# Performance work log

Measured on AMD Instinct MI355X. Metric: run time of the kernel, lower is better.

The kernel has to match this reference:

```python
import jax, jax.numpy as jnp
import numpy as np

# Decode-stage paged attention with ALiBi (HPU flat-PA style):
# batch2block scatter of queries, per-block QK + alibi bias, segment-wise
# stable softmax over each sequence's blocks, AV matmul, block2batch reduce.
BATCH = 32          # decode sequences
H = 32              # query heads
KVH = 8             # kv heads (GQA)
QPK = H // KVH      # queries per kv head
D = 128             # head size
BS = 128            # block size (tokens per KV-cache block)
BLOCKS_PER_SEQ = 16 # context 2048 tokens per sequence
U = BATCH * BLOCKS_PER_SEQ  # 512 used blocks
NB = 600            # total blocks in cache pool
SCALE = 1.0 / float(np.sqrt(D))
NEG = -1e30


def setup_inputs() -> dict:
    key = jax.random.key(0)
    k0, k1, k2 = jax.random.split(key, 3)
    query = jax.random.normal(k0, (BATCH, H, D), jnp.float32)
    key_cache = jax.random.normal(k1, (NB, BS, KVH, D), jnp.float32)
    value_cache = jax.random.normal(k2, (NB, BS, KVH, D), jnp.float32)
    # contiguous PA: used blocks are the first U blocks of the pool
    block_list = jnp.arange(U, dtype=jnp.int32)
    # each sequence owns BLOCKS_PER_SEQ consecutive blocks
    block_groups = (jnp.arange(U, dtype=jnp.int32) // BLOCKS_PER_SEQ).astype(jnp.int32)
    # all blocks fully used (context = BLOCKS_PER_SEQ*BS exactly)
    block_usage = jnp.full((U,), BS, dtype=jnp.int32)
    # alibi_blocks[u, p] = (global position) - (context_len - 1)  (<= 0)
    ctx = BLOCKS_PER_SEQ * BS
    pos = (jnp.arange(U) % BLOCKS_PER_SEQ)[:, None] * BS + jnp.arange(BS)[None, :]
    alibi_blocks = (pos - (ctx - 1)).astype(jnp.float32)
    # standard geometric alibi slopes: 2^(-8*(i+1)/H)
    alibi_slopes = 2.0 ** (-(jnp.arange(1, H + 1, dtype=jnp.float32)) * (8.0 / H))
    return dict(query=query, key_cache=key_cache, value_cache=value_cache,
                alibi_blocks=alibi_blocks, alibi_slopes=alibi_slopes,
                block_list=block_list, block_groups=block_groups,
                block_usage=block_usage)


def reference(query, key_cache, value_cache, alibi_blocks, alibi_slopes,
              block_list, block_groups, block_usage):
    # gather KV blocks from the paged cache
    K = key_cache[block_list]            # [U, BS, KVH, D]
    V = value_cache[block_list]          # [U, BS, KVH, D]
    # batch2block: replicate each sequence's query onto its blocks
    q = query[block_groups] * SCALE      # [U, H, D]
    qg = q.reshape(U, KVH, QPK, D)
    # QK^T per block (GQA: each kv head serves QPK query heads)
    scores = jnp.einsum('ugqd,ukgd->ugqk', qg, K).reshape(U, H, BS)
    # decode alibi bias: [U, H, BS] = alibi_blocks[:,None,:] * slopes[None,:,None]
    scores = scores + alibi_blocks[:, None, :] * alibi_slopes[None, :, None]
    # mask unused slots within each block
    valid = jnp.arange(BS, dtype=jnp.int32)[None, :] < block_usage[:, None]  # [U, BS]
    scores = jnp.where(valid[:, None, :], scores, NEG)
    # stable softmax across all blocks of each sequence (segment-wise)
    bmax = scores.max(-1)                                            # [U, H]
    gmax = jax.ops.segment_max(bmax, block_groups, num_segments=BATCH)
    e = jnp.exp(scores - gmax[block_groups][:, :, None])             # [U, H, BS]
    e = jnp.where(valid[:, None, :], e, 0.0)
    bsum = e.sum(-1)                                                 # [U, H]
    gsum = jax.ops.segment_sum(bsum, block_groups, num_segments=BATCH)  # [B, H]
    # AV per block, then block2batch reduce
    eg = e.reshape(U, KVH, QPK, BS)
    av = jnp.einsum('ugqk,ukgd->ugqd', eg, V).reshape(U, H, D)       # [U, H, D]
    out = jax.ops.segment_sum(av, block_groups, num_segments=BATCH)  # [B, H, D]
    out = out / gsum[:, :, None]
    return out.reshape(BATCH, H * D)
```

## Files before the change

kernel.cpp:

```cpp
#include <hip/hip_runtime.h>
#include <stdint.h>

#define BATCH 32
#define NH    32
#define KVH   8
#define QPK   4
#define DH    128
#define BS    128
#define NEG   (-1e30f)
#define SCALEF 0.08838834764831845f
#define MAXU  512

#define GAS __attribute__((address_space(1)))
#define LAS __attribute__((address_space(3)))

__global__ __launch_bounds__(256, 1)
void pa_alibi_decode(const float* __restrict__ query,
                     const float* __restrict__ key_cache,
                     const float* __restrict__ value_cache,
                     const float* __restrict__ alibi_blocks,
                     const float* __restrict__ alibi_slopes,
                     const int* __restrict__ block_list,
                     const int* __restrict__ block_groups,
                     const int* __restrict__ block_usage,
                     float* __restrict__ out,
                     int U) {
  __shared__ __align__(16) float Kbuf[4][2][32 * DH];
  __shared__ __align__(16) float q_lds[QPK * DH];
  __shared__ __align__(16) float p_lds[4][32 * QPK];
  __shared__ float combO[4][QPK][DH];
  __shared__ float combM[4][QPK];
  __shared__ float combS[4][QPK];
  __shared__ int   ulist[MAXU];
  __shared__ int   pblds[MAXU];
  __shared__ int   uslds[MAXU];
  __shared__ int   ucount;

  const int tid  = threadIdx.x;
  const int w    = tid >> 6;
  const int lane = tid & 63;
  const int r    = lane & 31;
  const int half = lane >> 5;
  const int b    = blockIdx.x >> 3;
  const int g    = blockIdx.x & 7;

  if (w == 0) {
    int cnt = 0;
    for (int base = 0; base < U; base += 64) {
      const int u = base + lane;
      const bool match = (u < U) && (block_groups[u] == b);
      const unsigned long long mk = __ballot(match);
      if (match) {
        const int pre = __popcll(mk & ((1ull << lane) - 1ull));
        ulist[cnt + pre] = u;
      }
      cnt += __popcll(mk);
    }
    if (lane == 0) ucount = cnt;
    for (int i = lane; i < cnt; i += 64) {
      const int u = ulist[i];
      pblds[i] = block_list[u];
      uslds[i] = block_usage[u];
    }
  }

  {
    const float* qsrc = query + ((size_t)b * NH + g * QPK) * DH;
    for (int e = tid; e < QPK * DH; e += 256) q_lds[e] = qsrc[e] * SCALEF;
  }

  float slope[QPK];
#pragma unroll
  for (int qh = 0; qh < QPK; ++qh) slope[qh] = alibi_slopes[g * QPK + qh];

  __syncthreads();

  const int nblk = ucount;

  float m[QPK], s[QPK], O[QPK][4];
#pragma unroll
  for (int qh = 0; qh < QPK; ++qh) {
    m[qh] = NEG; s[qh] = 0.f;
#pragma unroll
    for (int k = 0; k < 4; ++k) O[qh][k] = 0.f;
  }

  int cur = 0;
  int u_cur = 0, pb_cur = 0, us_cur = 0;
  if (nblk > 0) {
    u_cur = ulist[0]; pb_cur = pblds[0]; us_cur = uslds[0];
    const float* base = key_cache + ((size_t)pb_cur * BS + w * 32) * (KVH * DH) + (size_t)g * DH;
    float* buf = &Kbuf[w][0][0];
#pragma unroll
    for (int i = 0; i < 16; ++i) {
      const int t  = 2 * i + half;
      const int sg = r ^ t;
      __builtin_amdgcn_global_load_lds((const GAS void*)(base + (size_t)t * (KVH * DH) + sg * 4),
                                       (LAS void*)(buf + i * 256), 16, 0, 0);
    }
  }

  for (int c = 0; c < nblk; ++c) {
    __builtin_amdgcn_sched_barrier(0);
    asm volatile("s_waitcnt vmcnt(0)" ::: "memory");
    __builtin_amdgcn_sched_barrier(0);

    const float ab = alibi_blocks[(size_t)u_cur * BS + w * 32 + r];
    const bool has_nxt = (c + 1 < nblk);
    int u_nxt = 0, pb_nxt = 0, us_nxt = 0;
    if (has_nxt) { u_nxt = ulist[c + 1]; pb_nxt = pblds[c + 1]; us_nxt = uslds[c + 1]; }

    const float* vb = value_cache + ((size_t)pb_cur * BS + w * 32 + half) * (KVH * DH)
                    + (size_t)g * DH + r * 4;
    float4 vreg[16];
#pragma unroll
    for (int tp = 0; tp < 16; ++tp)
      vreg[tp] = *(const float4*)&vb[(size_t)tp * 2 * (KVH * DH)];

    if (has_nxt) {
      const float* base = key_cache + ((size_t)pb_nxt * BS + w * 32) * (KVH * DH) + (size_t)g * DH;
      float* buf = &Kbuf[w][cur ^ 1][0];
#pragma unroll
      for (int i = 0; i < 16; ++i) {
        const int t  = 2 * i + half;
        const int sg = r ^ t;
        __builtin_amdgcn_global_load_lds((const GAS void*)(base + (size_t)t * (KVH * DH) + sg * 4),
                                         (LAS void*)(buf + i * 256), 16, 0, 0);
      }
    }

    const float* kb = &Kbuf[w][cur][0];
    float acc[QPK] = {0.f, 0.f, 0.f, 0.f};
#pragma unroll
    for (int i = 0; i < 16; ++i) {
      const int j = half * 16 + i;
      const float4 kv = *(const float4*)&kb[r * DH + ((j ^ r) << 2)];
#pragma unroll
      for (int qh = 0; qh < QPK; ++qh) {
        const float4 qv = *(const float4*)&q_lds[qh * DH + (j << 2)];
        acc[qh] += kv.x * qv.x + kv.y * qv.y + kv.z * qv.z + kv.w * qv.w;
      }
    }

    const bool valid = (w * 32 + r) < us_cur;
    float p[QPK];
#pragma unroll
    for (int qh = 0; qh < QPK; ++qh) {
      float sc = acc[qh] + __shfl_xor(acc[qh], 32);
      sc += ab * slope[qh];
      if (!valid) sc = NEG;
      float cm = sc;
#pragma unroll
      for (int off = 1; off < 32; off <<= 1) cm = fmaxf(cm, __shfl_xor(cm, off));
      const float mnew = fmaxf(m[qh], cm);
      const float rs   = __expf(m[qh] - mnew);
      m[qh] = mnew;
      p[qh] = valid ? __expf(sc - mnew) : 0.f;
      s[qh] = s[qh] * rs + (half == 0 ? p[qh] : 0.f);
#pragma unroll
      for (int k = 0; k < 4; ++k) O[qh][k] *= rs;
    }
    if (half == 0)
      *(float4*)&p_lds[w][r * 4] = make_float4(p[0], p[1], p[2], p[3]);

#pragma unroll
    for (int tp = 0; tp < 16; ++tp) {
      const float4 pv = *(const float4*)&p_lds[w][(2 * tp + half) * 4];
      const float4 vv = vreg[tp];
      O[0][0] += pv.x * vv.x; O[0][1] += pv.x * vv.y; O[0][2] += pv.x * vv.z; O[0][3] += pv.x * vv.w;
      O[1][0] += pv.y * vv.x; O[1][1] += pv.y * vv.y; O[1][2] += pv.y * vv.z; O[1][3] += pv.y * vv.w;
      O[2][0] += pv.z * vv.x; O[2][1] += pv.z * vv.y; O[2][2] += pv.z * vv.z; O[2][3] += pv.z * vv.w;
      O[3][0] += pv.w * vv.x; O[3][1] += pv.w * vv.y; O[3][2] += pv.w * vv.z; O[3][3] += pv.w * vv.w;
    }

    u_cur = u_nxt; pb_cur = pb_nxt; us_cur = us_nxt;
    cur ^= 1;
  }

#pragma unroll
  for (int qh = 0; qh < QPK; ++qh) {
    float sv = s[qh];
#pragma unroll
    for (int off = 1; off < 64; off <<= 1) sv += __shfl_xor(sv, off);
#pragma unroll
    for (int k = 0; k < 4; ++k) O[qh][k] += __shfl_xor(O[qh][k], 32);
    if (half == 0) {
#pragma unroll
      for (int k = 0; k < 4; ++k) combO[w][qh][r * 4 + k] = O[qh][k];
    }
    if (lane == 0) { combM[w][qh] = m[qh]; combS[w][qh] = sv; }
  }
  __syncthreads();

  for (int e = tid; e < QPK * DH; e += 256) {
    const int qh = e >> 7;
    const int d  = e & 127;
    float M = combM[0][qh];
#pragma unroll
    for (int ww = 1; ww < 4; ++ww) M = fmaxf(M, combM[ww][qh]);
    float S = 0.f, Ov = 0.f;
#pragma unroll
    for (int ww = 0; ww < 4; ++ww) {
      const float f = __expf(combM[ww][qh] - M);
      S  += f * combS[ww][qh];
      Ov += f * combO[ww][qh][d];
    }
    out[((size_t)b * NH + g * QPK + qh) * DH + d] = Ov / S;
  }
}

extern "C" void kernel_launch(void* const* d_in, const int* in_sizes, int n_in,
                              void* d_out, int out_size, void* d_ws, size_t ws_size,
                              hipStream_t stream) {
  (void)n_in; (void)out_size; (void)d_ws; (void)ws_size;
  const float* query        = (const float*)d_in[0];
  const float* key_cache    = (const float*)d_in[1];
  const float* value_cache  = (const float*)d_in[2];
  const float* alibi_blocks = (const float*)d_in[3];
  const float* alibi_slopes = (const float*)d_in[4];
  const int*   block_list   = (const int*)d_in[5];
  const int*   block_groups = (const int*)d_in[6];
  const int*   block_usage  = (const int*)d_in[7];
  float*       out          = (float*)d_out;
  const int U = in_sizes[5];

  pa_alibi_decode<<<dim3(BATCH * KVH), dim3(256), 0, stream>>>(
      query, key_cache, value_cache, alibi_blocks, alibi_slopes,
      block_list, block_groups, block_usage, out, U);
}
```

Measured before the change: 118.4 us.

## Split each sequence's KV blocks across four workgroups with a combine kernel

The grid grows from 256 to 1024 workgroups by splitting each (batch, kv-head) pair's block list four ways. Each split writes partial max, sum and output to workspace, and a second kernel merges them with log-sum-exp rescaling. The LDS double-buffered K prefetch via global_load_lds is replaced by direct per-thread register loads of K. This aims to fill more of the GPU's compute units, at the cost of an extra launch, workspace traffic and no explicit prefetch overlap.

Result: slower. 141.9 us (+19.9%).

```diff
diff --git a/kernel.cpp b/kernel.cpp
--- a/kernel.cpp
+++ b/kernel.cpp
@@ -10,22 +10,20 @@
 #define NEG   (-1e30f)
 #define SCALEF 0.08838834764831845f
 #define MAXU  512
-
-#define GAS __attribute__((address_space(1)))
-#define LAS __attribute__((address_space(3)))
+#define SPLIT 4
 
 __global__ __launch_bounds__(256, 1)
-void pa_alibi_decode(const float* __restrict__ query,
-                     const float* __restrict__ key_cache,
-                     const float* __restrict__ value_cache,
-                     const float* __restrict__ alibi_blocks,
-                     const float* __restrict__ alibi_slopes,
-                     const int* __restrict__ block_list,
-                     const int* __restrict__ block_groups,
-                     const int* __restrict__ block_usage,
-                     float* __restrict__ out,
-                     int U) {
-  __shared__ __align__(16) float Kbuf[4][2][32 * DH];
+void pa_partial(const float* __restrict__ query,
+                const float* __restrict__ key_cache,
+                const float* __restrict__ value_cache,
+                const float* __restrict__ alibi_blocks,
+                const float* __restrict__ alibi_slopes,
+                const int* __restrict__ block_list,
+                const int* __restrict__ block_groups,
+                const int* __restrict__ block_usage,
+                float* __restrict__ Mp, float* __restrict__ Sp,
+                float* __restrict__ Op,
+                int U) {
   __shared__ __align__(16) float q_lds[QPK * DH];
   __shared__ __align__(16) float p_lds[4][32 * QPK];
   __shared__ float combO[4][QPK][DH];
@@ -41,8 +39,10 @@
   const int lane = tid & 63;
   const int r    = lane & 31;
   const int half = lane >> 5;
-  const int b    = blockIdx.x >> 3;
-  const int g    = blockIdx.x & 7;
+  const int bid  = blockIdx.x;
+  const int b    = bid >> 5;
+  const int g    = (bid >> 2) & 7;
+  const int s    = bid & 3;
 
   if (w == 0) {
     int cnt = 0;
@@ -77,72 +77,46 @@
 
   const int nblk = ucount;
 
-  float m[QPK], s[QPK], O[QPK][4];
+  float m[QPK], sacc[QPK], O[QPK][4];
 #pragma unroll
   for (int qh = 0; qh < QPK; ++qh) {
-    m[qh] = NEG; s[qh] = 0.f;
+    m[qh] = NEG; sacc[qh] = 0.f;
 #pragma unroll
     for (int k = 0; k < 4; ++k) O[qh][k] = 0.f;
   }
 
-  int cur = 0;
-  int u_cur = 0, pb_cur = 0, us_cur = 0;
-  if (nblk > 0) {
-    u_cur = ulist[0]; pb_cur = pblds[0]; us_cur = uslds[0];
-    const float* base = key_cache + ((size_t)pb_cur * BS + w * 32) * (KVH * DH) + (size_t)g * DH;
-    float* buf = &Kbuf[w][0][0];
-#pragma unroll
-    for (int i = 0; i < 16; ++i) {
-      const int t  = 2 * i + half;
-      const int sg = r ^ t;
-      __builtin_amdgcn_global_load_lds((const GAS void*)(base + (size_t)t * (KVH * DH) + sg * 4),
-                                       (LAS void*)(buf + i * 256), 16, 0, 0);
-    }
-  }
-
-  for (int c = 0; c < nblk; ++c) {
-    __builtin_amdgcn_sched_barrier(0);
-    asm volatile("s_waitcnt vmcnt(0)" ::: "memory");
-    __builtin_amdgcn_sched_barrier(0);
-
-    const float ab = alibi_blocks[(size_t)u_cur * BS + w * 32 + r];
-    const bool has_nxt = (c + 1 < nblk);
-    int u_nxt = 0, pb_nxt = 0, us_nxt = 0;
-    if (has_nxt) { u_nxt = ulist[c + 1]; pb_nxt = pblds[c + 1]; us_nxt = uslds[c + 1]; }
-
-    const float* vb = value_cache + ((size_t)pb_cur * BS + w * 32 + half) * (KVH * DH)
-                    + (size_t)g * DH + r * 4;
+  for (int i = s; i < nblk; i += SPLIT) {
+    const int u     = ulist[i];
+    const int pb    = pblds[i];
+    const int usage = uslds[i];
+
+    const float* kb = key_cache
+        + ((size_t)(pb * BS + w * 32 + r) * KVH + g) * DH + half * 64;
+    float4 kreg[16];
+#pragma unroll
+    for (int j = 0; j < 16; ++j) kreg[j] = *(const float4*)&kb[j * 4];
+
+    const float* vb = value_cache
+        + ((size_t)(pb * BS + w * 32 + half) * KVH + g) * DH + r * 4;
     float4 vreg[16];
 #pragma unroll
     for (int tp = 0; tp < 16; ++tp)
       vreg[tp] = *(const float4*)&vb[(size_t)tp * 2 * (KVH * DH)];
 
-    if (has_nxt) {
-      const float* base = key_cache + ((size_t)pb_nxt * BS + w * 32) * (KVH * DH) + (size_t)g * DH;
-      float* buf = &Kbuf[w][cur ^ 1][0];
-#pragma unroll
-      for (int i = 0; i < 16; ++i) {
-        const int t  = 2 * i + half;
-        const int sg = r ^ t;
-        __builtin_amdgcn_global_load_lds((const GAS void*)(base + (size_t)t * (KVH * DH) + sg * 4),
-                                         (LAS void*)(buf + i * 256), 16, 0, 0);
-      }
-    }
-
-    const float* kb = &Kbuf[w][cur][0];
+    const float ab = alibi_blocks[(size_t)u * BS + w * 32 + r];
+
     float acc[QPK] = {0.f, 0.f, 0.f, 0.f};
 #pragma unroll
-    for (int i = 0; i < 16; ++i) {
-      const int j = half * 16 + i;
-      const float4 kv = *(const float4*)&kb[r * DH + ((j ^ r) << 2)];
+    for (int j = 0; j < 16; ++j) {
+      const float4 kv = kreg[j];
 #pragma unroll
       for (int qh = 0; qh < QPK; ++qh) {
-        const float4 qv = *(const float4*)&q_lds[qh * DH + (j << 2)];
+        const float4 qv = *(const float4*)&q_lds[qh * DH + half * 64 + j * 4];
         acc[qh] += kv.x * qv.x + kv.y * qv.y + kv.z * qv.z + kv.w * qv.w;
       }
     }
 
-    const bool valid = (w * 32 + r) < us_cur;
+    const bool valid = (w * 32 + r) < usage;
     float p[QPK];
 #pragma unroll
     for (int qh = 0; qh < QPK; ++qh) {
@@ -156,7 +130,7 @@
       const float rs   = __expf(m[qh] - mnew);
       m[qh] = mnew;
       p[qh] = valid ? __expf(sc - mnew) : 0.f;
-      s[qh] = s[qh] * rs + (half == 0 ? p[qh] : 0.f);
+      sacc[qh] = sacc[qh] * rs + (half == 0 ? p[qh] : 0.f);
 #pragma unroll
       for (int k = 0; k < 4; ++k) O[qh][k] *= rs;
     }
@@ -172,14 +146,11 @@
       O[2][0] += pv.z * vv.x; O[2][1] += pv.z * vv.y; O[2][2] += pv.z * vv.z; O[2][3] += pv.z * vv.w;
       O[3][0] += pv.w * vv.x; O[3][1] += pv.w * vv.y; O[3][2] += pv.w * vv.z; O[3][3] += pv.w * vv.w;
     }
-
-    u_cur = u_nxt; pb_cur = pb_nxt; us_cur = us_nxt;
-    cur ^= 1;
   }
 
 #pragma unroll
   for (int qh = 0; qh < QPK; ++qh) {
-    float sv = s[qh];
+    float sv = sacc[qh];
 #pragma unroll
     for (int off = 1; off < 64; off <<= 1) sv += __shfl_xor(sv, off);
 #pragma unroll
@@ -205,14 +176,39 @@
       S  += f * combS[ww][qh];
       Ov += f * combO[ww][qh][d];
     }
-    out[((size_t)b * NH + g * QPK + qh) * DH + d] = Ov / S;
-  }
+    const int P = ((b * KVH + g) * QPK + qh) * SPLIT + s;
+    Op[(size_t)P * DH + d] = Ov;
+    if (d == 0) { Mp[P] = M; Sp[P] = S; }
+  }
+}
+
+__global__ __launch_bounds__(256, 1)
+void pa_combine(const float* __restrict__ Mp, const float* __restrict__ Sp,
+                const float* __restrict__ Op, float* __restrict__ out) {
+  const int e  = blockIdx.x * 256 + threadIdx.x;
+  const int b  = e >> 12;
+  const int h  = (e >> 7) & 31;
+  const int d  = e & 127;
+  const int g  = h >> 2;
+  const int qh = h & 3;
+  const int P  = ((b * KVH + g) * QPK + qh) * SPLIT;
+  float M = NEG;
+#pragma unroll
+  for (int s = 0; s < SPLIT; ++s) M = fmaxf(M, Mp[P + s]);
+  float S = 0.f, Ov = 0.f;
+#pragma unroll
+  for (int s = 0; s < SPLIT; ++s) {
+    const float f = __expf(Mp[P + s] - M);
+    S  += f * Sp[P + s];
+    Ov += f * Op[(size_t)(P + s) * DH + d];
+  }
+  out[e] = Ov / S;
 }
 
 extern "C" void kernel_launch(void* const* d_in, const int* in_sizes, int n_in,
                               void* d_out, int out_size, void* d_ws, size_t ws_size,
                               hipStream_t stream) {
-  (void)n_in; (void)out_size; (void)d_ws; (void)ws_size;
+  (void)n_in; (void)out_size; (void)ws_size;
   const float* query        = (const float*)d_in[0];
   const float* key_cache    = (const float*)d_in[1];
   const float* value_cache  = (const float*)d_in[2];
@@ -224,7 +220,14 @@
   float*       out          = (float*)d_out;
   const int U = in_sizes[5];
 
-  pa_alibi_decode<<<dim3(BATCH * KVH), dim3(256), 0, stream>>>(
+  const int NP = BATCH * KVH * QPK * SPLIT;
+  float* Mp = (float*)d_ws;
+  float* Sp = Mp + NP;
+  float* Op = Sp + NP;
+
+  pa_partial<<<dim3(BATCH * KVH * SPLIT), dim3(256), 0, stream>>>(
       query, key_cache, value_cache, alibi_blocks, alibi_slopes,
-      block_list, block_groups, block_usage, out, U);
+      block_list, block_groups, block_usage, Mp, Sp, Op, U);
+
+  pa_combine<<<dim3(BATCH * NH * DH / 256), dim3(256), 0, stream>>>(Mp, Sp, Op, out);
 }
```
